# Optimization experiments

Hardware: AMD Instinct MI355X
Metric: run time of the kernel (lower is better)

## Reference

```python
import jax, jax.numpy as jnp
import numpy as np

HIDDEN = 2048
NUM_EXPERTS = 8
TOP_K = 2
CAPACITY_FACTOR = 1.5
B, S = 2, 2048


def setup_inputs() -> dict:
    key = jax.random.key(0)
    k0, k1, k2 = jax.random.split(key, 3)
    hidden_states = jax.random.normal(k0, (B, S, HIDDEN), dtype=jnp.float32)
    # xavier-normal init per nn.init.xavier_normal_
    std1 = float(np.sqrt(2.0 / (HIDDEN + HIDDEN)))
    std2 = float(np.sqrt(2.0 / (HIDDEN + NUM_EXPERTS)))
    w1 = jax.random.normal(k1, (HIDDEN, HIDDEN), dtype=jnp.float32) * std1
    b1 = jnp.zeros((HIDDEN,), dtype=jnp.float32)
    w2 = jax.random.normal(k2, (NUM_EXPERTS, HIDDEN), dtype=jnp.float32) * std2
    b2 = jnp.zeros((NUM_EXPERTS,), dtype=jnp.float32)
    return {"hidden_states": hidden_states, "w1": w1, "b1": b1, "w2": w2, "b2": b2}


def reference(hidden_states, w1, b1, w2, b2):
    Bs, Ss, H = hidden_states.shape
    E, K = NUM_EXPERTS, TOP_K
    T = Bs * Ss
    capacity = int(T * CAPACITY_FACTOR * K / E)

    # router MLP: Linear -> ReLU -> Linear (dropout=0 -> identity)
    h = jax.nn.relu(jnp.einsum('bsh,oh->bso', hidden_states, w1) + b1)
    router_logits = jnp.einsum('bsh,eh->bse', h, w2) + b2  # [B,S,E]
    router_probs = jax.nn.softmax(router_logits, axis=-1)

    top_k_probs, top_k_indices = jax.lax.top_k(router_probs, K)  # [B,S,K]
    top_k_probs = top_k_probs / (jnp.sum(top_k_probs, axis=-1, keepdims=True) + 1e-8)

    # dispatch/combine: tokens claim capacity slots in (b,s,k) order.
    fe = top_k_indices.reshape(-1)            # [T*K] expert id per assignment
    fp = top_k_probs.reshape(-1)              # [T*K] prob per assignment
    onehot = (fe[:, None] == jnp.arange(E)[None, :]).astype(jnp.int32)  # [T*K,E]
    cum = jnp.cumsum(onehot, axis=0)          # running per-expert counts
    pos = jnp.take_along_axis(cum, fe[:, None], axis=1)[:, 0] - 1        # slot index
    valid = pos < capacity
    pos_c = jnp.minimum(pos, capacity - 1)
    tok = jnp.arange(T * K) // K              # flat token index

    dispatch = jnp.zeros((T, E, capacity), dtype=router_probs.dtype)
    combine = jnp.zeros((T, E, capacity), dtype=router_probs.dtype)
    dispatch = dispatch.at[tok, fe, pos_c].add(valid.astype(router_probs.dtype))
    combine = combine.at[tok, fe, pos_c].add(jnp.where(valid, fp, 0.0))
    dispatch_tensor = dispatch.reshape(Bs, Ss, E, capacity)
    combine_tensor = combine.reshape(Bs, Ss, E, capacity)

    # load-balancing aux loss
    router_prob_per_expert = jnp.mean(router_probs, axis=(0, 1))          # [E]
    expert_mask = jax.nn.one_hot(top_k_indices, E, dtype=router_probs.dtype)  # [B,S,K,E]
    expert_usage_rate = jnp.mean(expert_mask, axis=(0, 1, 2))             # [E]
    aux_loss = jnp.sum(router_prob_per_expert * expert_usage_rate) * E

    return dispatch_tensor, combine_tensor, router_probs, aux_loss
```

## Files before the change

kernel.cpp:

```cpp
#include <hip/hip_runtime.h>

#define HID   2048
#define NE    8
#define NK    2
#define NTOK  4096
#define NASS  (NTOK * NK)
#define CAP   1536
#define DISP_ELEMS ((size_t)NTOK * NE * CAP)
#define KBLK  (HID / 32)
#define NXBLK (NTOK * KBLK)
#define NPANEL 16
#define ZCHUNKS_PER_BLK 49152

typedef __bf16 bf16x8 __attribute__((ext_vector_type(8)));
typedef float  f32x4  __attribute__((ext_vector_type(4)));

typedef const __attribute__((address_space(1))) unsigned int GUint;
typedef       __attribute__((address_space(3))) unsigned int LUint;

__device__ __forceinline__ void gload16(const void* g, void* l) {
    __builtin_amdgcn_global_load_lds((GUint*)g, (LUint*)l, 16, 0, 0);
}

__global__ __launch_bounds__(256) void split_kernel(
    const float* __restrict__ X, const float* __restrict__ W1,
    __bf16* __restrict__ Xs, __bf16* __restrict__ Ws)
{
    int g = blockIdx.x * 256 + threadIdx.x;
    int blk = g >> 2, sub = g & 3;
    const float* s;
    __bf16* d;
    if (blk < NXBLK) { s = X  + (size_t)blk * 32 + sub * 8;
                       d = Xs + (size_t)blk * 64; }
    else             { s = W1 + (size_t)(blk - NXBLK) * 32 + sub * 8;
                       d = Ws + (size_t)(blk - NXBLK) * 64; }
    float x[8];
    float4 v0 = ((const float4*)s)[0], v1 = ((const float4*)s)[1];
    x[0]=v0.x; x[1]=v0.y; x[2]=v0.z; x[3]=v0.w;
    x[4]=v1.x; x[5]=v1.y; x[6]=v1.z; x[7]=v1.w;
    bf16x8 h8, l8;
#pragma unroll
    for (int j = 0; j < 8; ++j) {
        __bf16 h = (__bf16)x[j];
        h8[j] = h;
        l8[j] = (__bf16)(x[j] - (float)h);
    }
    *(bf16x8*)(d + sub * 8)      = h8;
    *(bf16x8*)(d + 32 + sub * 8) = l8;
}

__global__ __launch_bounds__(256, 3) void gemm1_mfma_kernel(
    const __bf16* __restrict__ Xs,
    const __bf16* __restrict__ Ws,
    const float* __restrict__ b1,
    const float* __restrict__ w2,
    float* __restrict__ partial,
    float* __restrict__ zout)
{
    __shared__ __bf16 As[128 * 64];
    __shared__ __bf16 Bs[128 * 64];
    __shared__ float  Part[2][64][2][NE];

    const int tid  = threadIdx.x;
    const int wid  = tid >> 6;
    const int lane = tid & 63;

    int wg  = blockIdx.x;
    int swz = (wg & 7) * 64 + (wg >> 3);
    const int bx = swz & 15;
    const int by = swz >> 4;
    const int brow = by * 128;
    const int bcol = bx * 128;

    const int srow   = lane >> 3;
    const int sslot  = lane & 7;

    const int wr = wid >> 1, wc = wid & 1;
    const int fr = lane & 15;
    const int fc = lane >> 4;

    f32x4* zdst = (f32x4*)zout + (size_t)blockIdx.x * ZCHUNKS_PER_BLK + tid;
    const f32x4 zz = (f32x4)0.f;

    f32x4 acc[4][4];
#pragma unroll
    for (int m = 0; m < 4; ++m)
#pragma unroll
        for (int n = 0; n < 4; ++n) acc[m][n] = (f32x4)0.f;

    for (int b = 0; b < KBLK; ++b) {
#pragma unroll
        for (int i = 0; i < 4; ++i) {
            int ra = wid * 32 + i * 8 + srow;
            int ca = sslot ^ (ra & 7);
            gload16(Xs + ((size_t)(brow + ra) * KBLK + b) * 64 + ca * 8,
                    &As[(wid * 32 + i * 8) * 64]);
            gload16(Ws + ((size_t)(bcol + ra) * KBLK + b) * 64 + ca * 8,
                    &Bs[(wid * 32 + i * 8) * 64]);
        }
        __syncthreads();

        {
            f32x4* z = zdst + (size_t)b * 768;
            __builtin_nontemporal_store(zz, z);
            __builtin_nontemporal_store(zz, z + 256);
            __builtin_nontemporal_store(zz, z + 512);
        }

        bf16x8 bh[4], bl[4];
#pragma unroll
        for (int n = 0; n < 4; ++n) {
            int rb = wc * 64 + n * 16 + fr;
            bh[n] = *(const bf16x8*)&Bs[rb * 64 + ((fc       ^ (rb & 7)) << 3)];
            bl[n] = *(const bf16x8*)&Bs[rb * 64 + (((4 + fc) ^ (rb & 7)) << 3)];
        }
#pragma unroll
        for (int m = 0; m < 4; ++m) {
            int ra = wr * 64 + m * 16 + fr;
            bf16x8 ah = *(const bf16x8*)&As[ra * 64 + ((fc       ^ (ra & 7)) << 3)];
            bf16x8 al = *(const bf16x8*)&As[ra * 64 + (((4 + fc) ^ (ra & 7)) << 3)];
#pragma unroll
            for (int n = 0; n < 4; ++n) {
                f32x4 c = acc[m][n];
                c = __builtin_amdgcn_mfma_f32_16x16x32_bf16(ah, bh[n], c, 0, 0, 0);
                c = __builtin_amdgcn_mfma_f32_16x16x32_bf16(al, bh[n], c, 0, 0, 0);
                c = __builtin_amdgcn_mfma_f32_16x16x32_bf16(ah, bl[n], c, 0, 0, 0);
                acc[m][n] = c;
            }
        }
        __syncthreads();
    }

    float w2v[NE][4], bias4[4];
#pragma unroll
    for (int n = 0; n < 4; ++n) {
        int col = bcol + wc * 64 + n * 16 + fr;
        bias4[n] = b1[col];
#pragma unroll
        for (int e = 0; e < NE; ++e) w2v[e][n] = w2[e * HID + col];
    }
#pragma unroll
    for (int m = 0; m < 4; ++m) {
#pragma unroll
        for (int j = 0; j < 4; ++j) {
            float esum[NE];
#pragma unroll
            for (int e = 0; e < NE; ++e) esum[e] = 0.f;
#pragma unroll
            for (int n = 0; n < 4; ++n) {
                float h = fmaxf(acc[m][n][j] + bias4[n], 0.f);
#pragma unroll
                for (int e = 0; e < NE; ++e) esum[e] += h * w2v[e][n];
            }
#pragma unroll
            for (int msk = 1; msk < 16; msk <<= 1)
#pragma unroll
                for (int e = 0; e < NE; ++e) esum[e] += __shfl_xor(esum[e], msk);
            if (fr == 0) {
                int row64 = m * 16 + fc * 4 + j;
#pragma unroll
                for (int e = 0; e < NE; ++e) Part[wr][row64][wc][e] = esum[e];
            }
        }
    }
    __syncthreads();
#pragma unroll
    for (int it = 0; it < 4; ++it) {
        int idx = it * 256 + tid;
        int row128 = idx >> 3, e = idx & 7;
        float v = Part[row128 >> 6][row128 & 63][0][e]
                + Part[row128 >> 6][row128 & 63][1][e];
        partial[((size_t)bx * NTOK + brow + row128) * NE + e] = v;
    }
}

__global__ __launch_bounds__(256) void logits_topk_kernel(
    const float* __restrict__ partial, const float* __restrict__ b2,
    float* __restrict__ probs_out, int* __restrict__ topk_e,
    float* __restrict__ topk_p)
{
    const int t = blockIdx.x * 256 + threadIdx.x;
    float lg[NE];
#pragma unroll
    for (int e = 0; e < NE; ++e) lg[e] = b2[e];
    for (int p = 0; p < NPANEL; ++p) {
        const float4* src = (const float4*)(partial + ((size_t)p * NTOK + t) * NE);
        float4 a = src[0], b = src[1];
        lg[0] += a.x; lg[1] += a.y; lg[2] += a.z; lg[3] += a.w;
        lg[4] += b.x; lg[5] += b.y; lg[6] += b.z; lg[7] += b.w;
    }
    float mx = -1e30f;
#pragma unroll
    for (int e = 0; e < NE; ++e) mx = fmaxf(mx, lg[e]);
    float sum = 0.f;
#pragma unroll
    for (int e = 0; e < NE; ++e) { lg[e] = expf(lg[e] - mx); sum += lg[e]; }
    float inv = 1.f / sum;
    float p[NE];
#pragma unroll
    for (int e = 0; e < NE; ++e) { p[e] = lg[e] * inv; probs_out[t * NE + e] = p[e]; }
    int e1 = 0;
#pragma unroll
    for (int e = 1; e < NE; ++e) if (p[e] > p[e1]) e1 = e;
    int e2 = -1;
#pragma unroll
    for (int e = 0; e < NE; ++e) if (e != e1 && (e2 < 0 || p[e] > p[e2])) e2 = e;
    float denom = p[e1] + p[e2] + 1e-8f;
    topk_e[t * NK + 0] = e1;
    topk_e[t * NK + 1] = e2;
    topk_p[t * NK + 0] = p[e1] / denom;
    topk_p[t * NK + 1] = p[e2] / denom;
}

__global__ __launch_bounds__(256) void finalize_kernel(
    const int* __restrict__ topk_e, const float* __restrict__ topk_p,
    const float* __restrict__ probs, float* __restrict__ dispatch,
    float* __restrict__ combine, float* __restrict__ aux_out)
{
    const int tid = threadIdx.x;
    __shared__ int   sc[256][NE];
    __shared__ float tot[NE];
    __shared__ float rps[256][NE];

    int cnt[NE];
#pragma unroll
    for (int e = 0; e < NE; ++e) cnt[e] = 0;
    const int base = tid * 32;
    int eloc[32];
    for (int i = 0; i < 32; ++i) { eloc[i] = topk_e[base + i]; cnt[eloc[i]]++; }
#pragma unroll
    for (int e = 0; e < NE; ++e) sc[tid][e] = cnt[e];
    __syncthreads();
    if (tid < NE) {
        int run = 0;
        for (int i = 0; i < 256; ++i) { int v = sc[i][tid]; sc[i][tid] = run; run += v; }
        tot[tid] = (float)run;
    }
    __syncthreads();
    int run[NE];
#pragma unroll
    for (int e = 0; e < NE; ++e) run[e] = sc[tid][e];
    for (int i = 0; i < 32; ++i) {
        const int a = base + i;
        const int e = eloc[i];
        const int p = run[e]++;
        if (p < CAP) {
            const int t = a >> 1;
            const size_t off = ((size_t)t * NE + e) * CAP + p;
            dispatch[off] = 1.0f;
            combine[off]  = topk_p[a];
        }
    }

    float ps[NE];
#pragma unroll
    for (int e = 0; e < NE; ++e) ps[e] = 0.f;
    for (int t = tid; t < NTOK; t += 256)
#pragma unroll
        for (int e = 0; e < NE; ++e) ps[e] += probs[t * NE + e];
#pragma unroll
    for (int e = 0; e < NE; ++e) rps[tid][e] = ps[e];
    __syncthreads();
    for (int s = 128; s > 0; s >>= 1) {
        if (tid < s) {
#pragma unroll
            for (int e = 0; e < NE; ++e) rps[tid][e] += rps[tid + s][e];
        }
        __syncthreads();
    }
    if (tid == 0) {
        float aux = 0.f;
#pragma unroll
        for (int e = 0; e < NE; ++e)
            aux += (rps[0][e] / (float)NTOK) * (tot[e] / (float)NASS);
        aux_out[0] = aux * (float)NE;
    }
}

extern "C" void kernel_launch(void* const* d_in, const int* in_sizes, int n_in,
                              void* d_out, int out_size, void* d_ws, size_t ws_size,
                              hipStream_t stream)
{
    const float* X  = (const float*)d_in[0];
    const float* w1 = (const float*)d_in[1];
    const float* b1 = (const float*)d_in[2];
    const float* w2 = (const float*)d_in[3];
    const float* b2 = (const float*)d_in[4];

    float* out      = (float*)d_out;
    float* dispatch = out;
    float* combine  = out + DISP_ELEMS;
    float* probs    = out + 2 * DISP_ELEMS;
    float* aux      = out + 2 * DISP_ELEMS + (size_t)NTOK * NE;

    __bf16* Xs      = (__bf16*)d_ws;
    __bf16* Ws      = Xs + (size_t)NTOK * HID * 2;
    float*  partial = (float*)(Ws + (size_t)HID * HID * 2);
    int*    topk_e  = (int*)(partial + (size_t)NPANEL * NTOK * NE);
    float*  topk_p  = (float*)(topk_e + NASS);

    split_kernel<<<((NTOK + HID) * KBLK * 4) / 256, 256, 0, stream>>>(X, w1, Xs, Ws);
    gemm1_mfma_kernel<<<512, 256, 0, stream>>>(Xs, Ws, b1, w2, partial, out);
    logits_topk_kernel<<<NTOK / 256, 256, 0, stream>>>(partial, b2, probs, topk_e, topk_p);
    finalize_kernel<<<1, 256, 0, stream>>>(topk_e, topk_p, probs, dispatch, combine, aux);
}
```

Measured before the change: 501.2 us.

## Double-buffer LDS tiles in router GEMM to overlap loads with MFMA

Splits the shared-memory A/B tiles into two buffers and prefetches the next K-block with global_load_lds while the current block is computed. A manual vmcnt wait and raw s_barrier replace __syncthreads so the prefetch stays in flight during the MFMA work. Doubling LDS lowers the launch-bounds occupancy hint from 3 to 2 blocks per CU. The last iteration issues a redundant wrapped load of block 0. The vmcnt(11) count has to match the number of outstanding loads and nontemporal stores exactly.

```diff
diff --git a/kernel.cpp b/kernel.cpp
--- a/kernel.cpp
+++ b/kernel.cpp
@@ -49,7 +49,7 @@
     *(bf16x8*)(d + 32 + sub * 8) = l8;
 }
 
-__global__ __launch_bounds__(256, 3) void gemm1_mfma_kernel(
+__global__ __launch_bounds__(256, 2) void gemm1_mfma_kernel(
     const __bf16* __restrict__ Xs,
     const __bf16* __restrict__ Ws,
     const float* __restrict__ b1,
@@ -57,8 +57,8 @@
     float* __restrict__ partial,
     float* __restrict__ zout)
 {
-    __shared__ __bf16 As[128 * 64];
-    __shared__ __bf16 Bs[128 * 64];
+    __shared__ __bf16 As[2][128 * 64];
+    __shared__ __bf16 Bs[2][128 * 64];
     __shared__ float  Part[2][64][2][NE];
 
     const int tid  = threadIdx.x;
@@ -88,37 +88,47 @@
 #pragma unroll
         for (int n = 0; n < 4; ++n) acc[m][n] = (f32x4)0.f;
 
+#define STAGE(buf, b)                                                          \
+    {                                                                          \
+        _Pragma("unroll")                                                      \
+        for (int i = 0; i < 4; ++i) {                                          \
+            int ra = wid * 32 + i * 8 + srow;                                  \
+            int ca = sslot ^ (ra & 7);                                         \
+            gload16(Xs + ((size_t)(brow + ra) * KBLK + (b)) * 64 + ca * 8,     \
+                    &As[buf][(wid * 32 + i * 8) * 64]);                        \
+            gload16(Ws + ((size_t)(bcol + ra) * KBLK + (b)) * 64 + ca * 8,     \
+                    &Bs[buf][(wid * 32 + i * 8) * 64]);                        \
+        }                                                                      \
+    }
+
+    STAGE(0, 0);
+
     for (int b = 0; b < KBLK; ++b) {
-#pragma unroll
-        for (int i = 0; i < 4; ++i) {
-            int ra = wid * 32 + i * 8 + srow;
-            int ca = sslot ^ (ra & 7);
-            gload16(Xs + ((size_t)(brow + ra) * KBLK + b) * 64 + ca * 8,
-                    &As[(wid * 32 + i * 8) * 64]);
-            gload16(Ws + ((size_t)(bcol + ra) * KBLK + b) * 64 + ca * 8,
-                    &Bs[(wid * 32 + i * 8) * 64]);
-        }
-        __syncthreads();
-
+        const int cur = b & 1;
+        STAGE(cur ^ 1, (b + 1) & (KBLK - 1));
         {
             f32x4* z = zdst + (size_t)b * 768;
             __builtin_nontemporal_store(zz, z);
             __builtin_nontemporal_store(zz, z + 256);
             __builtin_nontemporal_store(zz, z + 512);
         }
+        asm volatile("s_waitcnt vmcnt(11)" ::: "memory");
+        __builtin_amdgcn_sched_barrier(0);
+        __builtin_amdgcn_s_barrier();
+        __builtin_amdgcn_sched_barrier(0);
 
         bf16x8 bh[4], bl[4];
 #pragma unroll
         for (int n = 0; n < 4; ++n) {
             int rb = wc * 64 + n * 16 + fr;
-            bh[n] = *(const bf16x8*)&Bs[rb * 64 + ((fc       ^ (rb & 7)) << 3)];
-            bl[n] = *(const bf16x8*)&Bs[rb * 64 + (((4 + fc) ^ (rb & 7)) << 3)];
+            bh[n] = *(const bf16x8*)&Bs[cur][rb * 64 + ((fc       ^ (rb & 7)) << 3)];
+            bl[n] = *(const bf16x8*)&Bs[cur][rb * 64 + (((4 + fc) ^ (rb & 7)) << 3)];
         }
 #pragma unroll
         for (int m = 0; m < 4; ++m) {
             int ra = wr * 64 + m * 16 + fr;
-            bf16x8 ah = *(const bf16x8*)&As[ra * 64 + ((fc       ^ (ra & 7)) << 3)];
-            bf16x8 al = *(const bf16x8*)&As[ra * 64 + (((4 + fc) ^ (ra & 7)) << 3)];
+            bf16x8 ah = *(const bf16x8*)&As[cur][ra * 64 + ((fc       ^ (ra & 7)) << 3)];
+            bf16x8 al = *(const bf16x8*)&As[cur][ra * 64 + (((4 + fc) ^ (ra & 7)) << 3)];
 #pragma unroll
             for (int n = 0; n < 4; ++n) {
                 f32x4 c = acc[m][n];
@@ -128,7 +138,9 @@
                 acc[m][n] = c;
             }
         }
-        __syncthreads();
+        __builtin_amdgcn_sched_barrier(0);
+        __builtin_amdgcn_s_barrier();
+        __builtin_amdgcn_sched_barrier(0);
     }
 
     float w2v[NE][4], bias4[4];
@@ -172,6 +184,7 @@
                 + Part[row128 >> 6][row128 & 63][1][e];
         partial[((size_t)bx * NTOK + brow + row128) * NE + e] = v;
     }
+#undef STAGE
 }
 
 __global__ __launch_bounds__(256) void logits_topk_kernel(
```

Result: no change. 508.5 us (+1.4%).
